# Kernel optimization log

Hardware: AMD Instinct MI355X
Metric: run time of the kernel (lower is better)

Reference implementation:

```python
import jax, jax.numpy as jnp
import numpy as np

EPS = 1e-3
LOG2PI = float(np.log(2.0 * np.pi))

# dims
B, Z, Y, T, D = 32768, 256, 32, 64, 4  # batch, z_dim, y_dim, n_types, type_dim


def setup_inputs() -> dict:
    key = jax.random.key(0)
    ks = jax.random.split(key, 8)
    z = jax.random.normal(ks[0], (B, Z), dtype=jnp.float32)
    batch_x = jax.random.normal(ks[1], (B, T, D), dtype=jnp.float32)
    miss_list = jax.random.randint(ks[2], (B, T), 0, 2, dtype=jnp.int32)  # 1=observed, 0=missing
    data_mean = jax.random.normal(ks[3], (T, D), dtype=jnp.float32)
    data_var = jax.random.uniform(ks[4], (T, D), dtype=jnp.float32, minval=0.5, maxval=1.5)
    # weights init N(0, 0.005) as in the torch module; biases zero
    Wy = jax.random.normal(ks[5], (T * Y, Z), dtype=jnp.float32) * 0.005
    by = jnp.zeros((T * Y,), dtype=jnp.float32)
    Wm = jax.random.normal(ks[6], (T, D, Y), dtype=jnp.float32) * 0.005
    bm = jnp.zeros((T, D), dtype=jnp.float32)
    Wv = jax.random.normal(ks[7], (T, D, Y), dtype=jnp.float32) * 0.005
    bv = jnp.zeros((T, D), dtype=jnp.float32)
    return {"z": z, "batch_x": batch_x, "miss_list": miss_list,
            "data_mean": data_mean, "data_var": data_var,
            "Wy": Wy, "by": by, "Wm": Wm, "bm": bm, "Wv": Wv, "bv": bv}


def reference(z, batch_x, miss_list, data_mean, data_var, Wy, by, Wm, bm, Wv, bv):
    # y_layer: z -> [B, T*Y], grouped into per-type gamma slices [B, T, Y]
    y = z @ Wy.T + by
    gamma = y.reshape(y.shape[0], T, Y)

    mask = miss_list.astype(gamma.dtype)            # [B, T], 1=observed
    m3 = mask[:, :, None]                           # [B, T, 1]

    # per-type tiny linears (dynamic_partition + Linear + dynamic_stitch).
    # Numerically: same linear on all rows; missing rows are under no_grad,
    # realized here as stop_gradient on the missing partition.
    lin_m = jnp.einsum('bty,tdy->btd', gamma, Wm) + bm   # [B, T, D]
    lin_v = jnp.einsum('bty,tdy->btd', gamma, Wv) + bv
    est_mean = m3 * lin_m + (1.0 - m3) * jax.lax.stop_gradient(lin_m)
    est_var_raw = m3 * lin_v + (1.0 - m3) * jax.lax.stop_gradient(lin_v)

    # loglik_real: softplus variance, denormalize with data mean/var
    dvar = jnp.clip(data_var, EPS)
    est_var = jnp.clip(jax.nn.softplus(est_var_raw), EPS, 1e20)
    mean_x = jnp.sqrt(dvar) * est_mean + data_mean       # [B, T, D]
    var_x = dvar * est_var                               # [B, T, D]

    log_p = -0.5 * jnp.sum((batch_x - mean_x) ** 2 / var_x + jnp.log(var_x) + LOG2PI, axis=-1)  # [B, T]
    log_p_x = log_p * mask
    log_p_x_missing = log_p * (1.0 - mask)
    return (log_p_x, log_p_x_missing, mean_x, var_x)
```

## Files before the change

### kernel.cpp

```cpp
#include <hip/hip_runtime.h>


#define Bsz   32768
#define Tsz   64
#define Dsz   4
#define Ysz   32
#define Zsz   256
#define Nsz   512
#define BTtot (Bsz * Tsz)
#define EPS_  1e-3f
#define LOG2PI_ 1.8378770664093453f

#define BM       32
#define NT       512
#define ASTRIDE  264
#define LSTRIDE  524

typedef __attribute__((ext_vector_type(4))) float  f32x4;
typedef __attribute__((ext_vector_type(8))) short  short8;
typedef __attribute__((ext_vector_type(2))) unsigned int uint2v;

static __device__ __forceinline__ unsigned short f2bf(float f) {
    unsigned int u = __float_as_uint(f);
    return (unsigned short)((u + 0x7fffu + ((u >> 16) & 1u)) >> 16);
}
static __device__ __forceinline__ float bf2f(unsigned short h) {
    return __uint_as_float(((unsigned int)h) << 16);
}
static __device__ __forceinline__ unsigned int cvt_pk_bf16(float a, float b) {
    unsigned int r;
    asm("v_cvt_pk_bf16_f32 %0, %1, %2" : "=v"(r) : "v"(a), "v"(b));
    return r;
}

__global__ __launch_bounds__(256)
void hidec_prep(const float* __restrict__ Wy, const float* __restrict__ by,
                const float* __restrict__ Wm, const float* __restrict__ bm,
                const float* __restrict__ Wv, const float* __restrict__ bv,
                unsigned short* __restrict__ weff, float* __restrict__ beff) {
    __shared__ float Ml[8][Ysz];
    __shared__ float byl[Ysz];
    const int t   = blockIdx.x;
    const int tid = threadIdx.x;
    {
        int j = tid >> 5, y = tid & 31;
        const float* src = (j < 4) ? Wm : Wv;
        Ml[j][y] = src[(t * Dsz + (j & 3)) * Ysz + y];
    }
    if (tid < Ysz) byl[tid] = by[t * Ysz + tid];
    __syncthreads();

    const int k = tid;
    const int kk = k >> 5, q = (k >> 3) & 3, je = k & 7;
    float wy[Ysz];
#pragma unroll
    for (int y = 0; y < Ysz; ++y)
        wy[y] = Wy[(size_t)(t * Ysz + y) * Zsz + k];
#pragma unroll
    for (int j = 0; j < 8; ++j) {
        float acc = 0.f;
#pragma unroll
        for (int y = 0; y < Ysz; ++y) acc = fmaf(Ml[j][y], wy[y], acc);
        int n   = t * 8 + j;
        int tau = n >> 4, c = n & 15;
        weff[((((tau * 8 + kk) * 4 + q) * 16 + c) * 8) + je] = f2bf(acc);
    }
    if (tid < 8) {
        int d = tid & 3;
        float s = ((tid < 4) ? bm : bv)[t * Dsz + d];
        for (int y = 0; y < Ysz; ++y) s = fmaf(byl[y], Ml[tid][y], s);
        beff[t * 8 + tid] = s;
    }
}

__global__ __launch_bounds__(NT, 4)
void hidec_main(const float* __restrict__ z, const float* __restrict__ bx,
                const int* __restrict__ miss, const float* __restrict__ dmean,
                const float* __restrict__ dvarp, const unsigned short* __restrict__ weff,
                const float* __restrict__ beff, float* __restrict__ out) {
    __shared__ unsigned short buf[BM * LSTRIDE];

    const int tid  = threadIdx.x;
    const long row0 = (long)blockIdx.x * BM;

    unsigned short* a_lds = buf;
#pragma unroll
    for (int i = 0; i < 4; ++i) {
        int idx4 = tid + i * NT;
        int r  = idx4 >> 6;
        int c4 = idx4 & 63;
        float4 v = *(const float4*)(z + (row0 + r) * Zsz + c4 * 4);
        uint2v pk;
        pk.x = cvt_pk_bf16(v.x, v.y);
        pk.y = cvt_pk_bf16(v.z, v.w);
        *(uint2v*)&a_lds[r * ASTRIDE + c4 * 4] = pk;
    }
    __syncthreads();

    const int lane = tid & 63;
    const int w    = tid >> 6;
    const int c    = lane & 15;
    const int q    = lane >> 4;

    f32x4 acc[8];
#pragma unroll
    for (int i = 0; i < 8; ++i) acc[i] = (f32x4){0.f, 0.f, 0.f, 0.f};

    const unsigned short* wp = weff + ((size_t)(w * 4) * 8) * 512 + lane * 8;

#pragma unroll
    for (int kk = 0; kk < 8; ++kk) {
        short8 b0 = *(const short8*)(wp + kk * 512 + 0 * 4096);
        short8 b1 = *(const short8*)(wp + kk * 512 + 1 * 4096);
        short8 b2 = *(const short8*)(wp + kk * 512 + 2 * 4096);
        short8 b3 = *(const short8*)(wp + kk * 512 + 3 * 4096);
        short8 a0 = *(const short8*)&a_lds[(0 * 16 + c) * ASTRIDE + kk * 32 + q * 8];
        short8 a1 = *(const short8*)&a_lds[(1 * 16 + c) * ASTRIDE + kk * 32 + q * 8];
        acc[0] = __builtin_amdgcn_mfma_f32_16x16x32_bf16(a0, b0, acc[0], 0, 0, 0);
        acc[1] = __builtin_amdgcn_mfma_f32_16x16x32_bf16(a1, b0, acc[1], 0, 0, 0);
        acc[2] = __builtin_amdgcn_mfma_f32_16x16x32_bf16(a0, b1, acc[2], 0, 0, 0);
        acc[3] = __builtin_amdgcn_mfma_f32_16x16x32_bf16(a1, b1, acc[3], 0, 0, 0);
        acc[4] = __builtin_amdgcn_mfma_f32_16x16x32_bf16(a0, b2, acc[4], 0, 0, 0);
        acc[5] = __builtin_amdgcn_mfma_f32_16x16x32_bf16(a1, b2, acc[5], 0, 0, 0);
        acc[6] = __builtin_amdgcn_mfma_f32_16x16x32_bf16(a0, b3, acc[6], 0, 0, 0);
        acc[7] = __builtin_amdgcn_mfma_f32_16x16x32_bf16(a1, b3, acc[7], 0, 0, 0);
    }

    const int t = lane;
    float4 dv4 = *(const float4*)(dvarp + t * 4);
    float4 dm4 = *(const float4*)(dmean + t * 4);
    float4 xp[4];
    int    mp[4];
#pragma unroll
    for (int pp = 0; pp < 4; ++pp) {
        long bt = (row0 + pp * 8 + w) * Tsz + t;
        xp[pp] = *(const float4*)(bx + bt * 4);
        mp[pp] = miss[bt];
    }
    float bb[4];
#pragma unroll
    for (int ti = 0; ti < 4; ++ti) bb[ti] = beff[w * 64 + ti * 16 + c];

#pragma unroll
    for (int pp = 0; pp < 4; ++pp) {
        asm volatile("" : "+v"(xp[pp].x), "+v"(xp[pp].y),
                          "+v"(xp[pp].z), "+v"(xp[pp].w), "+v"(mp[pp]));
    }
    asm volatile("" : "+v"(dv4.x), "+v"(dv4.y), "+v"(dv4.z), "+v"(dv4.w),
                      "+v"(dm4.x), "+v"(dm4.y), "+v"(dm4.z), "+v"(dm4.w));
    asm volatile("" : "+v"(bb[0]), "+v"(bb[1]), "+v"(bb[2]), "+v"(bb[3]));

    __syncthreads();

    unsigned short* lin = buf;
#pragma unroll
    for (int h = 0; h < 2; ++h) {
#pragma unroll
        for (int ti = 0; ti < 4; ++ti) {
            int cb = w * 64 + ti * 16 + c;
            const f32x4 a = acc[ti * 2 + h];
            unsigned int p01 = cvt_pk_bf16(a[0] + bb[ti], a[1] + bb[ti]);
            unsigned int p23 = cvt_pk_bf16(a[2] + bb[ti], a[3] + bb[ti]);
            int rbase = h * 16 + q * 4;
            lin[(rbase + 0) * LSTRIDE + cb] = (unsigned short)(p01 & 0xffffu);
            lin[(rbase + 1) * LSTRIDE + cb] = (unsigned short)(p01 >> 16);
            lin[(rbase + 2) * LSTRIDE + cb] = (unsigned short)(p23 & 0xffffu);
            lin[(rbase + 3) * LSTRIDE + cb] = (unsigned short)(p23 >> 16);
        }
    }
    __syncthreads();

    float dca[4] = {fmaxf(dv4.x, EPS_), fmaxf(dv4.y, EPS_),
                    fmaxf(dv4.z, EPS_), fmaxf(dv4.w, EPS_)};
    float sqa[4] = {sqrtf(dca[0]), sqrtf(dca[1]), sqrtf(dca[2]), sqrtf(dca[3])};
    float dma[4] = {dm4.x, dm4.y, dm4.z, dm4.w};
    float sldv = __logf(dca[0]) + __logf(dca[1]) + __logf(dca[2]) + __logf(dca[3]);

#pragma unroll
    for (int pp = 0; pp < 4; ++pp) {
        int rl  = pp * 8 + w;
        long bt = (row0 + rl) * Tsz + t;

        short8 l8 = *(const short8*)&lin[rl * LSTRIDE + t * 8];
        float lm[4], lv[4];
#pragma unroll
        for (int d = 0; d < 4; ++d) {
            lm[d] = bf2f((unsigned short)l8[d]);
            lv[d] = bf2f((unsigned short)l8[4 + d]);
        }

        float mk = (float)mp[pp];
        float xa[4] = {xp[pp].x, xp[pp].y, xp[pp].z, xp[pp].w};

        float mean_o[4], var_o[4];
        float s = sldv;
        float evp = 1.f;
#pragma unroll
        for (int d = 0; d < 4; ++d) {
            float mean = fmaf(sqa[d], lm[d], dma[d]);
            float v    = lv[d];
            float sp   = fmaxf(v, 0.f) + __logf(1.f + __expf(-fabsf(v)));
            float ev   = fminf(fmaxf(sp, EPS_), 1e20f);
            float var  = dca[d] * ev;
            float diff = xa[d] - mean;
            s = fmaf(diff * diff, __builtin_amdgcn_rcpf(var), s);
            evp *= ev;
            mean_o[d] = mean;
            var_o[d]  = var;
        }
        s += __logf(evp);
        float logp = -0.5f * (s + 4.f * LOG2PI_);

        float lx = logp * mk;
        out[bt]         = lx;
        out[BTtot + bt] = logp - lx;

        *(float4*)(out + 2L * BTtot + bt * 4) =
            (float4){mean_o[0], mean_o[1], mean_o[2], mean_o[3]};
        *(float4*)(out + 6L * BTtot + bt * 4) =
            (float4){var_o[0], var_o[1], var_o[2], var_o[3]};
    }
}

extern "C" void kernel_launch(void* const* d_in, const int* in_sizes, int n_in,
                              void* d_out, int out_size, void* d_ws, size_t ws_size,
                              hipStream_t stream) {
    const float* z     = (const float*)d_in[0];
    const float* bx    = (const float*)d_in[1];
    const int*   miss  = (const int*)d_in[2];
    const float* dmean = (const float*)d_in[3];
    const float* dvar  = (const float*)d_in[4];
    const float* Wy    = (const float*)d_in[5];
    const float* by    = (const float*)d_in[6];
    const float* Wm    = (const float*)d_in[7];
    const float* bm    = (const float*)d_in[8];
    const float* Wv    = (const float*)d_in[9];
    const float* bv    = (const float*)d_in[10];
    float* out = (float*)d_out;

    unsigned short* weff = (unsigned short*)d_ws;
    float* beff = (float*)((char*)d_ws + (size_t)Nsz * Zsz * 2);

    hidec_prep<<<Tsz, Zsz, 0, stream>>>(Wy, by, Wm, bm, Wv, bv, weff, beff);
    hidec_main<<<Bsz / BM, NT, 0, stream>>>(z, bx, miss, dmean, dvar, weff, beff, out);
}
```

Baseline: 175.5 us.

## Split fused kernel into GEMM and elementwise post kernels via workspace buffer

Splits the fused GEMM-plus-loglik kernel into two kernels. The GEMM kernel writes bias-added bf16 linear outputs to a workspace buffer in a packed layout, and a separate lightweight post kernel reads them along with batch_x and the mask to compute the outputs. The aim is to drop the LDS round-trip and the second barrier, and to let each kernel keep its own occupancy and launch shape. The cost is an extra 32 MB write and read through global memory plus one more launch. The old fused kernel is kept as a fallback when the workspace is too small.

Result: slower. 184.6 us (+5.2%).

```diff
diff --git a/kernel.cpp b/kernel.cpp
--- a/kernel.cpp
+++ b/kernel.cpp
@@ -15,6 +15,8 @@
 #define NT       512
 #define ASTRIDE  264
 #define LSTRIDE  524
+#define LINP_OFF 524288
+#define LINP_BYTES ((size_t)Bsz * Nsz * 2)
 
 typedef __attribute__((ext_vector_type(4))) float  f32x4;
 typedef __attribute__((ext_vector_type(8))) short  short8;
@@ -74,16 +76,13 @@
 }
 
 __global__ __launch_bounds__(NT, 4)
-void hidec_main(const float* __restrict__ z, const float* __restrict__ bx,
-                const int* __restrict__ miss, const float* __restrict__ dmean,
-                const float* __restrict__ dvarp, const unsigned short* __restrict__ weff,
-                const float* __restrict__ beff, float* __restrict__ out) {
-    __shared__ unsigned short buf[BM * LSTRIDE];
+void hidec_gemm(const float* __restrict__ z, const unsigned short* __restrict__ weff,
+                const float* __restrict__ beff, unsigned short* __restrict__ linp) {
+    __shared__ unsigned short a_lds[BM * ASTRIDE];
 
     const int tid  = threadIdx.x;
     const long row0 = (long)blockIdx.x * BM;
 
-    unsigned short* a_lds = buf;
 #pragma unroll
     for (int i = 0; i < 4; ++i) {
         int idx4 = tid + i * NT;
@@ -95,12 +94,17 @@
         pk.y = cvt_pk_bf16(v.z, v.w);
         *(uint2v*)&a_lds[r * ASTRIDE + c4 * 4] = pk;
     }
-    __syncthreads();
 
     const int lane = tid & 63;
     const int w    = tid >> 6;
     const int c    = lane & 15;
     const int q    = lane >> 4;
+
+    float bb[4];
+#pragma unroll
+    for (int ti = 0; ti < 4; ++ti) bb[ti] = beff[w * 64 + ti * 16 + c];
+
+    __syncthreads();
 
     f32x4 acc[8];
 #pragma unroll
@@ -126,50 +130,46 @@
         acc[7] = __builtin_amdgcn_mfma_f32_16x16x32_bf16(a1, b3, acc[7], 0, 0, 0);
     }
 
-    const int t = lane;
+#pragma unroll
+    for (int h = 0; h < 2; ++h) {
+#pragma unroll
+        for (int ti = 0; ti < 4; ++ti) {
+            const f32x4 a = acc[ti * 2 + h];
+            uint2v pk;
+            pk.x = cvt_pk_bf16(a[0] + bb[ti], a[1] + bb[ti]);
+            pk.y = cvt_pk_bf16(a[2] + bb[ti], a[3] + bb[ti]);
+            size_t unit = ((size_t)blockIdx.x * 8 + h * 4 + q) * 512
+                        + (w * 64 + ti * 16 + c);
+            *(uint2v*)(linp + unit * 4) = pk;
+        }
+    }
+}
+
+__global__ __launch_bounds__(256)
+void hidec_post(const float* __restrict__ bx, const int* __restrict__ miss,
+                const float* __restrict__ dmean, const float* __restrict__ dvarp,
+                const unsigned short* __restrict__ linp, float* __restrict__ out) {
+    const int tid = threadIdx.x;
+    const int t   = tid & 63;
+    const long rq = (long)blockIdx.x * 4 + (tid >> 6);
+
+    const unsigned short* lp = linp + rq * 2048 + t * 32;
+    short8 u01 = *(const short8*)(lp +  0);
+    short8 u23 = *(const short8*)(lp +  8);
+    short8 u45 = *(const short8*)(lp + 16);
+    short8 u67 = *(const short8*)(lp + 24);
+
+    float4 xq[4];
+    int    mq[4];
+#pragma unroll
+    for (int r = 0; r < 4; ++r) {
+        long bt = (rq * 4 + r) * Tsz + t;
+        xq[r] = *(const float4*)(bx + bt * 4);
+        mq[r] = miss[bt];
+    }
+
     float4 dv4 = *(const float4*)(dvarp + t * 4);
     float4 dm4 = *(const float4*)(dmean + t * 4);
-    float4 xp[4];
-    int    mp[4];
-#pragma unroll
-    for (int pp = 0; pp < 4; ++pp) {
-        long bt = (row0 + pp * 8 + w) * Tsz + t;
-        xp[pp] = *(const float4*)(bx + bt * 4);
-        mp[pp] = miss[bt];
-    }
-    float bb[4];
-#pragma unroll
-    for (int ti = 0; ti < 4; ++ti) bb[ti] = beff[w * 64 + ti * 16 + c];
-
-#pragma unroll
-    for (int pp = 0; pp < 4; ++pp) {
-        asm volatile("" : "+v"(xp[pp].x), "+v"(xp[pp].y),
-                          "+v"(xp[pp].z), "+v"(xp[pp].w), "+v"(mp[pp]));
-    }
-    asm volatile("" : "+v"(dv4.x), "+v"(dv4.y), "+v"(dv4.z), "+v"(dv4.w),
-                      "+v"(dm4.x), "+v"(dm4.y), "+v"(dm4.z), "+v"(dm4.w));
-    asm volatile("" : "+v"(bb[0]), "+v"(bb[1]), "+v"(bb[2]), "+v"(bb[3]));
-
-    __syncthreads();
-
-    unsigned short* lin = buf;
-#pragma unroll
-    for (int h = 0; h < 2; ++h) {
-#pragma unroll
-        for (int ti = 0; ti < 4; ++ti) {
-            int cb = w * 64 + ti * 16 + c;
-            const f32x4 a = acc[ti * 2 + h];
-            unsigned int p01 = cvt_pk_bf16(a[0] + bb[ti], a[1] + bb[ti]);
-            unsigned int p23 = cvt_pk_bf16(a[2] + bb[ti], a[3] + bb[ti]);
-            int rbase = h * 16 + q * 4;
-            lin[(rbase + 0) * LSTRIDE + cb] = (unsigned short)(p01 & 0xffffu);
-            lin[(rbase + 1) * LSTRIDE + cb] = (unsigned short)(p01 >> 16);
-            lin[(rbase + 2) * LSTRIDE + cb] = (unsigned short)(p23 & 0xffffu);
-            lin[(rbase + 3) * LSTRIDE + cb] = (unsigned short)(p23 >> 16);
-        }
-    }
-    __syncthreads();
-
     float dca[4] = {fmaxf(dv4.x, EPS_), fmaxf(dv4.y, EPS_),
                     fmaxf(dv4.z, EPS_), fmaxf(dv4.w, EPS_)};
     float sqa[4] = {sqrtf(dca[0]), sqrtf(dca[1]), sqrtf(dca[2]), sqrtf(dca[3])};
@@ -177,20 +177,21 @@
     float sldv = __logf(dca[0]) + __logf(dca[1]) + __logf(dca[2]) + __logf(dca[3]);
 
 #pragma unroll
-    for (int pp = 0; pp < 4; ++pp) {
-        int rl  = pp * 8 + w;
-        long bt = (row0 + rl) * Tsz + t;
-
-        short8 l8 = *(const short8*)&lin[rl * LSTRIDE + t * 8];
+    for (int r = 0; r < 4; ++r) {
+        long bt = (rq * 4 + r) * Tsz + t;
+
         float lm[4], lv[4];
-#pragma unroll
-        for (int d = 0; d < 4; ++d) {
-            lm[d] = bf2f((unsigned short)l8[d]);
-            lv[d] = bf2f((unsigned short)l8[4 + d]);
-        }
-
-        float mk = (float)mp[pp];
-        float xa[4] = {xp[pp].x, xp[pp].y, xp[pp].z, xp[pp].w};
+        lm[0] = bf2f((unsigned short)u01[r]);
+        lm[1] = bf2f((unsigned short)u01[4 + r]);
+        lm[2] = bf2f((unsigned short)u23[r]);
+        lm[3] = bf2f((unsigned short)u23[4 + r]);
+        lv[0] = bf2f((unsigned short)u45[r]);
+        lv[1] = bf2f((unsigned short)u45[4 + r]);
+        lv[2] = bf2f((unsigned short)u67[r]);
+        lv[3] = bf2f((unsigned short)u67[4 + r]);
+
+        float mk = (float)mq[r];
+        float xa[4] = {xq[r].x, xq[r].y, xq[r].z, xq[r].w};
 
         float mean_o[4], var_o[4];
         float s = sldv;
@@ -215,6 +216,150 @@
         out[bt]         = lx;
         out[BTtot + bt] = logp - lx;
 
+        *(float4*)(out + 2L * BTtot + bt * 4) =
+            (float4){mean_o[0], mean_o[1], mean_o[2], mean_o[3]};
+        *(float4*)(out + 6L * BTtot + bt * 4) =
+            (float4){var_o[0], var_o[1], var_o[2], var_o[3]};
+    }
+}
+
+__global__ __launch_bounds__(NT, 4)
+void hidec_fused(const float* __restrict__ z, const float* __restrict__ bx,
+                 const int* __restrict__ miss, const float* __restrict__ dmean,
+                 const float* __restrict__ dvarp, const unsigned short* __restrict__ weff,
+                 const float* __restrict__ beff, float* __restrict__ out) {
+    __shared__ unsigned short buf[BM * LSTRIDE];
+    const int tid  = threadIdx.x;
+    const long row0 = (long)blockIdx.x * BM;
+
+    unsigned short* a_lds = buf;
+#pragma unroll
+    for (int i = 0; i < 4; ++i) {
+        int idx4 = tid + i * NT;
+        int r  = idx4 >> 6;
+        int c4 = idx4 & 63;
+        float4 v = *(const float4*)(z + (row0 + r) * Zsz + c4 * 4);
+        uint2v pk;
+        pk.x = cvt_pk_bf16(v.x, v.y);
+        pk.y = cvt_pk_bf16(v.z, v.w);
+        *(uint2v*)&a_lds[r * ASTRIDE + c4 * 4] = pk;
+    }
+    __syncthreads();
+
+    const int lane = tid & 63;
+    const int w    = tid >> 6;
+    const int c    = lane & 15;
+    const int q    = lane >> 4;
+
+    f32x4 acc[8];
+#pragma unroll
+    for (int i = 0; i < 8; ++i) acc[i] = (f32x4){0.f, 0.f, 0.f, 0.f};
+
+    const unsigned short* wp = weff + ((size_t)(w * 4) * 8) * 512 + lane * 8;
+#pragma unroll
+    for (int kk = 0; kk < 8; ++kk) {
+        short8 b0 = *(const short8*)(wp + kk * 512 + 0 * 4096);
+        short8 b1 = *(const short8*)(wp + kk * 512 + 1 * 4096);
+        short8 b2 = *(const short8*)(wp + kk * 512 + 2 * 4096);
+        short8 b3 = *(const short8*)(wp + kk * 512 + 3 * 4096);
+        short8 a0 = *(const short8*)&a_lds[(0 * 16 + c) * ASTRIDE + kk * 32 + q * 8];
+        short8 a1 = *(const short8*)&a_lds[(1 * 16 + c) * ASTRIDE + kk * 32 + q * 8];
+        acc[0] = __builtin_amdgcn_mfma_f32_16x16x32_bf16(a0, b0, acc[0], 0, 0, 0);
+        acc[1] = __builtin_amdgcn_mfma_f32_16x16x32_bf16(a1, b0, acc[1], 0, 0, 0);
+        acc[2] = __builtin_amdgcn_mfma_f32_16x16x32_bf16(a0, b1, acc[2], 0, 0, 0);
+        acc[3] = __builtin_amdgcn_mfma_f32_16x16x32_bf16(a1, b1, acc[3], 0, 0, 0);
+        acc[4] = __builtin_amdgcn_mfma_f32_16x16x32_bf16(a0, b2, acc[4], 0, 0, 0);
+        acc[5] = __builtin_amdgcn_mfma_f32_16x16x32_bf16(a1, b2, acc[5], 0, 0, 0);
+        acc[6] = __builtin_amdgcn_mfma_f32_16x16x32_bf16(a0, b3, acc[6], 0, 0, 0);
+        acc[7] = __builtin_amdgcn_mfma_f32_16x16x32_bf16(a1, b3, acc[7], 0, 0, 0);
+    }
+
+    const int t = lane;
+    float4 dv4 = *(const float4*)(dvarp + t * 4);
+    float4 dm4 = *(const float4*)(dmean + t * 4);
+    float4 xp[4];
+    int    mp[4];
+#pragma unroll
+    for (int pp = 0; pp < 4; ++pp) {
+        long bt = (row0 + pp * 8 + w) * Tsz + t;
+        xp[pp] = *(const float4*)(bx + bt * 4);
+        mp[pp] = miss[bt];
+    }
+    float bb[4];
+#pragma unroll
+    for (int ti = 0; ti < 4; ++ti) bb[ti] = beff[w * 64 + ti * 16 + c];
+#pragma unroll
+    for (int pp = 0; pp < 4; ++pp) {
+        asm volatile("" : "+v"(xp[pp].x), "+v"(xp[pp].y),
+                          "+v"(xp[pp].z), "+v"(xp[pp].w), "+v"(mp[pp]));
+    }
+    asm volatile("" : "+v"(dv4.x), "+v"(dv4.y), "+v"(dv4.z), "+v"(dv4.w),
+                      "+v"(dm4.x), "+v"(dm4.y), "+v"(dm4.z), "+v"(dm4.w));
+    asm volatile("" : "+v"(bb[0]), "+v"(bb[1]), "+v"(bb[2]), "+v"(bb[3]));
+
+    __syncthreads();
+
+    unsigned short* lin = buf;
+#pragma unroll
+    for (int h = 0; h < 2; ++h) {
+#pragma unroll
+        for (int ti = 0; ti < 4; ++ti) {
+            int cb = w * 64 + ti * 16 + c;
+            const f32x4 a = acc[ti * 2 + h];
+            unsigned int p01 = cvt_pk_bf16(a[0] + bb[ti], a[1] + bb[ti]);
+            unsigned int p23 = cvt_pk_bf16(a[2] + bb[ti], a[3] + bb[ti]);
+            int rbase = h * 16 + q * 4;
+            lin[(rbase + 0) * LSTRIDE + cb] = (unsigned short)(p01 & 0xffffu);
+            lin[(rbase + 1) * LSTRIDE + cb] = (unsigned short)(p01 >> 16);
+            lin[(rbase + 2) * LSTRIDE + cb] = (unsigned short)(p23 & 0xffffu);
+            lin[(rbase + 3) * LSTRIDE + cb] = (unsigned short)(p23 >> 16);
+        }
+    }
+    __syncthreads();
+
+    float dca[4] = {fmaxf(dv4.x, EPS_), fmaxf(dv4.y, EPS_),
+                    fmaxf(dv4.z, EPS_), fmaxf(dv4.w, EPS_)};
+    float sqa[4] = {sqrtf(dca[0]), sqrtf(dca[1]), sqrtf(dca[2]), sqrtf(dca[3])};
+    float dma[4] = {dm4.x, dm4.y, dm4.z, dm4.w};
+    float sldv = __logf(dca[0]) + __logf(dca[1]) + __logf(dca[2]) + __logf(dca[3]);
+
+#pragma unroll
+    for (int pp = 0; pp < 4; ++pp) {
+        int rl  = pp * 8 + w;
+        long bt = (row0 + rl) * Tsz + t;
+
+        short8 l8 = *(const short8*)&lin[rl * LSTRIDE + t * 8];
+        float lm[4], lv[4];
+#pragma unroll
+        for (int d = 0; d < 4; ++d) {
+            lm[d] = bf2f((unsigned short)l8[d]);
+            lv[d] = bf2f((unsigned short)l8[4 + d]);
+        }
+        float mk = (float)mp[pp];
+        float xa[4] = {xp[pp].x, xp[pp].y, xp[pp].z, xp[pp].w};
+
+        float mean_o[4], var_o[4];
+        float s = sldv;
+        float evp = 1.f;
+#pragma unroll
+        for (int d = 0; d < 4; ++d) {
+            float mean = fmaf(sqa[d], lm[d], dma[d]);
+            float v    = lv[d];
+            float sp   = fmaxf(v, 0.f) + __logf(1.f + __expf(-fabsf(v)));
+            float ev   = fminf(fmaxf(sp, EPS_), 1e20f);
+            float var  = dca[d] * ev;
+            float diff = xa[d] - mean;
+            s = fmaf(diff * diff, __builtin_amdgcn_rcpf(var), s);
+            evp *= ev;
+            mean_o[d] = mean;
+            var_o[d]  = var;
+        }
+        s += __logf(evp);
+        float logp = -0.5f * (s + 4.f * LOG2PI_);
+
+        float lx = logp * mk;
+        out[bt]         = lx;
+        out[BTtot + bt] = logp - lx;
         *(float4*)(out + 2L * BTtot + bt * 4) =
             (float4){mean_o[0], mean_o[1], mean_o[2], mean_o[3]};
         *(float4*)(out + 6L * BTtot + bt * 4) =
@@ -242,5 +387,13 @@
     float* beff = (float*)((char*)d_ws + (size_t)Nsz * Zsz * 2);
 
     hidec_prep<<<Tsz, Zsz, 0, stream>>>(Wy, by, Wm, bm, Wv, bv, weff, beff);
-    hidec_main<<<Bsz / BM, NT, 0, stream>>>(z, bx, miss, dmean, dvar, weff, beff, out);
-}
+
+    if (ws_size >= (size_t)LINP_OFF + LINP_BYTES) {
+        unsigned short* linp = (unsigned short*)((char*)d_ws + LINP_OFF);
+        hidec_gemm<<<Bsz / BM, NT, 0, stream>>>(z, weff, beff, linp);
+        hidec_post<<<Bsz / 4 / 4, 256, 0, stream>>>(bx, miss, dmean, dvar, linp, out);
+    } else {
+        hidec_fused<<<Bsz / BM, NT, 0, stream>>>(z, bx, miss, dmean, dvar,
+                                                 weff, beff, out);
+    }
+}
```
